# Performance work log

Measured on AMD Instinct MI355X. Metric: run time of the kernel, lower is better.

The kernel has to match this reference:

```python
import jax, jax.numpy as jnp
import numpy as np

D_MODEL = 768
HEAD = 12
D_K = D_MODEL // HEAD


def setup_inputs() -> dict:
    key = jax.random.key(0)
    ks = jax.random.split(key, 9)
    s = 1.0 / np.sqrt(D_MODEL)
    return {
        "x": jax.random.normal(ks[0], (2, 4096, D_MODEL), dtype=jnp.float32),
        "Wq": jax.random.normal(ks[1], (D_MODEL, D_MODEL), dtype=jnp.float32) * s,
        "bq": jax.random.normal(ks[2], (D_MODEL,), dtype=jnp.float32) * 0.01,
        "Wk": jax.random.normal(ks[3], (D_MODEL, D_MODEL), dtype=jnp.float32) * s,
        "bk": jax.random.normal(ks[4], (D_MODEL,), dtype=jnp.float32) * 0.01,
        "Wv": jax.random.normal(ks[5], (D_MODEL, D_MODEL), dtype=jnp.float32) * s,
        "bv": jax.random.normal(ks[6], (D_MODEL,), dtype=jnp.float32) * 0.01,
        "Wo": jax.random.normal(ks[7], (D_MODEL, D_MODEL), dtype=jnp.float32) * s,
        "bo": jax.random.normal(ks[8], (D_MODEL,), dtype=jnp.float32) * 0.01,
    }


def reference(x, Wq, bq, Wk, bk, Wv, bv, Wo, bo):
    B, S, _ = x.shape
    # Linear projections, split into heads: [B, H, S, d_k]
    def proj(W, b):
        return (x @ W + b).reshape(B, S, HEAD, D_K).transpose(0, 2, 1, 3)
    Q, K, V = proj(Wq, bq), proj(Wk, bk), proj(Wv, bv)
    scale = 1.0 / jnp.sqrt(jnp.asarray(D_K, x.dtype))
    # [B, H, S, S] attention scores (materialized, as in the original module)
    scores = jnp.einsum('bhqd,bhkd->bhqk', Q, K) * scale
    probs = jax.nn.softmax(scores, axis=-1)  # dropout is identity in eval mode
    ctx = jnp.einsum('bhqk,bhkd->bhqd', probs, V)
    ctx = ctx.transpose(0, 2, 1, 3).reshape(B, S, D_MODEL)
    return ctx @ Wo + bo
```

## Files before the change

### kernel.cpp

```cpp
#include <hip/hip_runtime.h>

#define D_MODEL 768
#define S_LEN   4096
#define NHEAD   12
#define DK      64
#define TKA     64

typedef _Float16 f16;
typedef _Float16 f16x8 __attribute__((ext_vector_type(8)));
typedef _Float16 f16x4 __attribute__((ext_vector_type(4)));
typedef __fp16   fp16x2 __attribute__((ext_vector_type(2)));
typedef float    f32x4 __attribute__((ext_vector_type(4)));

#define MFMA16(a, b, c) __builtin_amdgcn_mfma_f32_16x16x32_f16(a, b, c, 0, 0, 0)

#define Q_PRESCALE 0.18033688f
#define SOFTMAX_C  11.54156036f

__device__ inline f16x8 ldf(const f16* p) {
    return *reinterpret_cast<const f16x8*>(p);
}

__device__ inline void gl2lds16(const f16* g, f16* l) {
    __builtin_amdgcn_global_load_lds(
        (const __attribute__((address_space(1))) void*)g,
        (__attribute__((address_space(3))) void*)l, 16, 0, 0);
}

__global__ __launch_bounds__(256) void cvt_x_kernel(const float* __restrict__ x,
                                                    f16* __restrict__ xb) {
    size_t i = ((size_t)blockIdx.x * 256 + threadIdx.x) * 4;
    float4 v = *reinterpret_cast<const float4*>(x + i);
    f16x4 o = { (f16)v.x, (f16)v.y, (f16)v.z, (f16)v.w };
    *reinterpret_cast<f16x4*>(xb + i) = o;
}

__global__ __launch_bounds__(256) void wtrans_kernel(const float* __restrict__ Wq,
                                                     const float* __restrict__ Wk,
                                                     const float* __restrict__ Wv,
                                                     const float* __restrict__ Wo,
                                                     f16* __restrict__ WT) {
    const int z = blockIdx.z;
    const float* in = (z == 0) ? Wq : (z == 1) ? Wk : (z == 2) ? Wv : Wo;
    f16* out = WT + (size_t)z * D_MODEL * D_MODEL;
    __shared__ float tile[32][33];
    const int tx = threadIdx.x, ty = threadIdx.y;
    const int n0 = blockIdx.x * 32, k0 = blockIdx.y * 32;
#pragma unroll
    for (int j = 0; j < 32; j += 8)
        tile[ty + j][tx] = in[(size_t)(k0 + ty + j) * D_MODEL + n0 + tx];
    __syncthreads();
#pragma unroll
    for (int j = 0; j < 32; j += 8)
        out[(size_t)(n0 + ty + j) * D_MODEL + k0 + tx] = (f16)tile[tx][ty + j];
}

__global__ __launch_bounds__(256, 3) void gemm_qkv_kernel(
        const f16* __restrict__ A, const f16* __restrict__ WT,
        const float* __restrict__ bq, const float* __restrict__ bk,
        const float* __restrict__ bv,
        f16* __restrict__ Qb, f16* __restrict__ Kb, f16* __restrict__ Vt) {
    __shared__ __align__(16) f16 asmem[3][128 * 32];
    __shared__ __align__(16) f16 bsmem[3][128 * 32];
    const int z = blockIdx.z;
    const f16* Bt = WT + (size_t)z * D_MODEL * D_MODEL;
    const float* bias = (z == 0) ? bq : (z == 1) ? bk : bv;
    const int w = threadIdx.x >> 6;
    const int lane = threadIdx.x & 63;
    const int ln = lane & 15, quad = lane >> 4;
    const int mb = blockIdx.x * 128;
    const int nb = blockIdx.y * 128;
    const int mloc = (w & 1) * 64, nloc = (w >> 1) * 64;
    const int l0 = w * 64 + lane;

    auto stage = [&](int buf, int kb) {
#pragma unroll
        for (int p = 0; p < 2; p++) {
            const int l = p * 256 + l0;
            gl2lds16(A + (size_t)(mb + (l >> 2)) * D_MODEL + kb + (l & 3) * 8,
                     &asmem[buf][(p * 256 + w * 64) * 8]);
        }
#pragma unroll
        for (int p = 0; p < 2; p++) {
            const int l = p * 256 + l0;
            gl2lds16(Bt + (size_t)(nb + (l >> 2)) * D_MODEL + kb + (l & 3) * 8,
                     &bsmem[buf][(p * 256 + w * 64) * 8]);
        }
    };

    f32x4 acc[4][4] = {};
    stage(0, 0);
    stage(1, 32);
    __syncthreads();

    const int NIT = D_MODEL / 32;
    int cb = 0, sb = 2;
    for (int it = 0; it < NIT; ++it) {
        f16x8 af[4], bf[4];
#pragma unroll
        for (int i = 0; i < 4; i++)
            af[i] = ldf(&asmem[cb][(mloc + i * 16 + ln) * 32 + quad * 8]);
#pragma unroll
        for (int t = 0; t < 4; t++)
            bf[t] = ldf(&bsmem[cb][(nloc + t * 16 + ln) * 32 + quad * 8]);
#pragma unroll
        for (int i = 0; i < 4; i++)
#pragma unroll
            for (int t = 0; t < 4; t++)
                acc[i][t] = MFMA16(af[i], bf[t], acc[i][t]);
        __syncthreads();
        if (it + 2 < NIT) stage(sb, (it + 2) * 32);
        cb = (cb == 2) ? 0 : cb + 1;
        sb = (sb == 2) ? 0 : sb + 1;
    }

#pragma unroll
    for (int t = 0; t < 4; t++) {
        const int n = nb + nloc + t * 16 + ln;
        const float bval = bias[n];
        const int h = n >> 6, d = n & 63;
#pragma unroll
        for (int i = 0; i < 4; i++) {
            const int m = mb + mloc + i * 16 + quad * 4;
            const int b = m >> 12, s = m & 4095;
            const int bh = b * NHEAD + h;
            if (z == 0) {
#pragma unroll
                for (int r = 0; r < 4; r++)
                    Qb[((size_t)bh * S_LEN + s + r) * DK + d] =
                        (f16)((acc[i][t][r] + bval) * Q_PRESCALE);
            } else if (z == 1) {
#pragma unroll
                for (int r = 0; r < 4; r++)
                    Kb[((size_t)bh * S_LEN + s + r) * DK + d] =
                        (f16)(acc[i][t][r] + bval);
            } else {
                f16x4 pk;
#pragma unroll
                for (int r = 0; r < 4; r++) pk[r] = (f16)(acc[i][t][r] + bval);
                *reinterpret_cast<f16x4*>(&Vt[((size_t)bh * DK + d) * S_LEN + s]) = pk;
            }
        }
    }
}

__global__ __launch_bounds__(256, 3) void attn_kernel(const f16* __restrict__ Qb,
                                                      const f16* __restrict__ Kb,
                                                      const f16* __restrict__ Vt,
                                                      f16* __restrict__ Ctx) {
    __shared__ __align__(16) f16 kbuf[3][TKA * DK];
    __shared__ __align__(16) f16 vbuf[3][DK * TKA];

    const int w = threadIdx.x >> 6;
    const int lane = threadIdx.x & 63;
    const int ln = lane & 15, quad = lane >> 4;

    const int blk = blockIdx.x;
    const int xcd = blk & 7, sidx = blk >> 3;
    const int bh = xcd * 3 + (sidx >> 5);
    const int qb = (sidx & 31) * 128;
    const int b = bh / NHEAD, h = bh % NHEAD;

    const f16* Kbh = Kb + (size_t)bh * S_LEN * DK;
    const f16* Vbh = Vt + (size_t)bh * DK * S_LEN;

    f16x8 aq[2][2];
#pragma unroll
    for (int i2 = 0; i2 < 2; i2++) {
        const f16* qp = Qb + ((size_t)bh * S_LEN + qb + w * 32 + i2 * 16 + ln) * DK;
        aq[i2][0] = ldf(qp + quad * 8);
        aq[i2][1] = ldf(qp + 32 + quad * 8);
    }

    int rS[2], ckS[2], cvS[2];
#pragma unroll
    for (int p = 0; p < 2; p++) {
        const int l = p * 256 + w * 64 + lane;
        const int r = l >> 3;
        rS[p]  = r;
        ckS[p] = ((l & 7) - r - (r >> 2)) & 7;
        cvS[p] = ((l & 7) - r - (r >> 3)) & 7;
    }

    auto stage = [&](int buf, int kk) {
#pragma unroll
        for (int p = 0; p < 2; p++)
            gl2lds16(Kbh + (size_t)(kk + rS[p]) * DK + ckS[p] * 8,
                     &kbuf[buf][(p * 256 + w * 64) * 8]);
#pragma unroll
        for (int p = 0; p < 2; p++)
            gl2lds16(Vbh + (size_t)rS[p] * S_LEN + kk + cvS[p] * 8,
                     &vbuf[buf][(p * 256 + w * 64) * 8]);
    };

    f32x4 acc[4][2] = {};
    float lsum[2] = {0.f, 0.f};

    stage(0, 0);
    stage(1, TKA);
    __syncthreads();

    const int NIT = S_LEN / TKA;
    int cb = 0, sb = 2;
    for (int it = 0; it < NIT; ++it) {
        const f16* kb = kbuf[cb];
        const f16* vb = vbuf[cb];

        union { f16x8 v; fp16x2 h2[4]; } pb[2][2];

#pragma unroll
        for (int kt = 0; kt < 2; kt++) {
#pragma unroll
            for (int a = 0; a < 2; a++) {
                const int rr = kt * 32 + 8 * (ln >> 2) + 4 * a + (ln & 3);
                const int sw = rr + (rr >> 2);
                const f16x8 kf0 = ldf(kb + rr * DK + (((quad + sw) & 7) * 8));
                const f16x8 kf1 = ldf(kb + rr * DK + (((quad + 4 + sw) & 7) * 8));
#pragma unroll
                for (int i2 = 0; i2 < 2; i2++) {
                    f32x4 si = { -SOFTMAX_C, -SOFTMAX_C, -SOFTMAX_C, -SOFTMAX_C };
                    si = MFMA16(kf0, aq[i2][0], si);
                    si = MFMA16(kf1, aq[i2][1], si);
                    const float e0 = __builtin_amdgcn_exp2f(si[0]);
                    const float e1 = __builtin_amdgcn_exp2f(si[1]);
                    const float e2 = __builtin_amdgcn_exp2f(si[2]);
                    const float e3 = __builtin_amdgcn_exp2f(si[3]);
                    lsum[i2] += (e0 + e1) + (e2 + e3);
                    pb[kt][i2].h2[2 * a]     = __builtin_amdgcn_cvt_pkrtz(e0, e1);
                    pb[kt][i2].h2[2 * a + 1] = __builtin_amdgcn_cvt_pkrtz(e2, e3);
                }
            }
        }

#pragma unroll
        for (int t = 0; t < 4; t++) {
            const int rr = t * 16 + ln;
            const int sw = rr + (rr >> 3);
#pragma unroll
            for (int kt = 0; kt < 2; kt++) {
                const f16x8 vf = ldf(vb + rr * TKA + (((quad + 4 * kt + sw) & 7) * 8));
#pragma unroll
                for (int i2 = 0; i2 < 2; i2++)
                    acc[t][i2] = MFMA16(vf, pb[kt][i2].v, acc[t][i2]);
            }
        }

        __syncthreads();
        if (it + 2 < NIT) stage(sb, (it + 2) * TKA);
        cb = (cb == 2) ? 0 : cb + 1;
        sb = (sb == 2) ? 0 : sb + 1;
    }

#pragma unroll
    for (int i2 = 0; i2 < 2; i2++) {
        float l = lsum[i2];
        l += __shfl_xor(l, 16, 64);
        l += __shfl_xor(l, 32, 64);
        const float rl = 1.0f / l;
        const int q = qb + w * 32 + i2 * 16 + ln;
        f16* cp = Ctx + ((size_t)b * S_LEN + q) * D_MODEL + h * DK + 4 * quad;
#pragma unroll
        for (int t = 0; t < 4; t++) {
            f16x4 pk;
#pragma unroll
            for (int r = 0; r < 4; r++) pk[r] = (f16)(acc[t][i2][r] * rl);
            *reinterpret_cast<f16x4*>(cp + t * 16) = pk;
        }
    }
}

__global__ __launch_bounds__(256, 3) void gemm_o_kernel(const f16* __restrict__ A,
                                                        const f16* __restrict__ Bt,
                                                        const float* __restrict__ bo,
                                                        float* __restrict__ out) {
    __shared__ __align__(16) f16 asmem[3][128 * 32];
    __shared__ __align__(16) f16 bsmem[3][128 * 32];
    const int w = threadIdx.x >> 6;
    const int lane = threadIdx.x & 63;
    const int ln = lane & 15, quad = lane >> 4;
    const int mb = blockIdx.x * 128;
    const int nb = blockIdx.y * 128;
    const int mloc = (w & 1) * 64, nloc = (w >> 1) * 64;
    const int l0 = w * 64 + lane;

    auto stage = [&](int buf, int kb) {
#pragma unroll
        for (int p = 0; p < 2; p++) {
            const int l = p * 256 + l0;
            gl2lds16(A + (size_t)(mb + (l >> 2)) * D_MODEL + kb + (l & 3) * 8,
                     &asmem[buf][(p * 256 + w * 64) * 8]);
        }
#pragma unroll
        for (int p = 0; p < 2; p++) {
            const int l = p * 256 + l0;
            gl2lds16(Bt + (size_t)(nb + (l >> 2)) * D_MODEL + kb + (l & 3) * 8,
                     &bsmem[buf][(p * 256 + w * 64) * 8]);
        }
    };

    f32x4 acc[4][4] = {};
    stage(0, 0);
    stage(1, 32);
    __syncthreads();

    const int NIT = D_MODEL / 32;
    int cb = 0, sb = 2;
    for (int it = 0; it < NIT; ++it) {
        f16x8 af[4], bf[4];
#pragma unroll
        for (int i = 0; i < 4; i++)
            af[i] = ldf(&asmem[cb][(mloc + i * 16 + ln) * 32 + quad * 8]);
#pragma unroll
        for (int t = 0; t < 4; t++)
            bf[t] = ldf(&bsmem[cb][(nloc + t * 16 + ln) * 32 + quad * 8]);
#pragma unroll
        for (int i = 0; i < 4; i++)
#pragma unroll
            for (int t = 0; t < 4; t++)
                acc[i][t] = MFMA16(af[i], bf[t], acc[i][t]);
        __syncthreads();
        if (it + 2 < NIT) stage(sb, (it + 2) * 32);
        cb = (cb == 2) ? 0 : cb + 1;
        sb = (sb == 2) ? 0 : sb + 1;
    }

#pragma unroll
    for (int t = 0; t < 4; t++) {
        const int n = nb + nloc + t * 16 + ln;
        const float bval = bo[n];
#pragma unroll
        for (int i = 0; i < 4; i++) {
            const int m = mb + mloc + i * 16 + quad * 4;
#pragma unroll
            for (int r = 0; r < 4; r++)
                out[(size_t)(m + r) * D_MODEL + n] = acc[i][t][r] + bval;
        }
    }
}

extern "C" void kernel_launch(void* const* d_in, const int* in_sizes, int n_in,
                              void* d_out, int out_size, void* d_ws, size_t ws_size,
                              hipStream_t stream) {
    const float* x  = (const float*)d_in[0];
    const float* Wq = (const float*)d_in[1];
    const float* bq = (const float*)d_in[2];
    const float* Wk = (const float*)d_in[3];
    const float* bk = (const float*)d_in[4];
    const float* Wv = (const float*)d_in[5];
    const float* bv = (const float*)d_in[6];
    const float* Wo = (const float*)d_in[7];
    const float* bo = (const float*)d_in[8];
    float* out = (float*)d_out;

    f16* ws = (f16*)d_ws;
    f16* Xb  = ws;
    f16* Ctx = ws;
    f16* WT  = ws + 6291456;
    f16* Qb  = ws + 8650752;
    f16* Kb  = ws + 14942208;
    f16* Vt  = ws + 21233664;

    cvt_x_kernel<<<6144, 256, 0, stream>>>(x, Xb);
    wtrans_kernel<<<dim3(24, 24, 4), dim3(32, 8), 0, stream>>>(Wq, Wk, Wv, Wo, WT);
    gemm_qkv_kernel<<<dim3(64, 6, 3), 256, 0, stream>>>(Xb, WT, bq, bk, bv, Qb, Kb, Vt);
    attn_kernel<<<768, 256, 0, stream>>>(Qb, Kb, Vt, Ctx);
    gemm_o_kernel<<<dim3(64, 6), 256, 0, stream>>>(Ctx, WT + (size_t)3 * D_MODEL * D_MODEL, bo, out);
}
```

Baseline: 271.3 us.

## Switch to double-buffered LDS with static buffers and precomputed offsets

Replaces the triple-buffered LDS ring in the QKV GEMM, attention and output GEMM kernels with a double buffer. The loop is unrolled by two so buffer indices become compile-time constants, and global and LDS address offsets are precomputed outside the loop. The attention kernel also raises wave priority around the PV MFMAs and accumulates the row sum with packed float2 adds, and the QKV GEMM raises its occupancy hint to 4 blocks. The aim is less LDS and fewer registers so more blocks fit per CU, plus less per-iteration address arithmetic. The cost is a shorter prefetch distance: the next tile is issued only after a barrier, right after the previous compute, which may expose more memory latency.

```diff
diff --git a/kernel.cpp b/kernel.cpp
--- a/kernel.cpp
+++ b/kernel.cpp
@@ -11,6 +11,7 @@
 typedef _Float16 f16x4 __attribute__((ext_vector_type(4)));
 typedef __fp16   fp16x2 __attribute__((ext_vector_type(2)));
 typedef float    f32x4 __attribute__((ext_vector_type(4)));
+typedef float    f32x2 __attribute__((ext_vector_type(2)));
 
 #define MFMA16(a, b, c) __builtin_amdgcn_mfma_f32_16x16x32_f16(a, b, c, 0, 0, 0)
 
@@ -55,13 +56,13 @@
         out[(size_t)(n0 + ty + j) * D_MODEL + k0 + tx] = (f16)tile[tx][ty + j];
 }
 
-__global__ __launch_bounds__(256, 3) void gemm_qkv_kernel(
+__global__ __launch_bounds__(256, 4) void gemm_qkv_kernel(
         const f16* __restrict__ A, const f16* __restrict__ WT,
         const float* __restrict__ bq, const float* __restrict__ bk,
         const float* __restrict__ bv,
         f16* __restrict__ Qb, f16* __restrict__ Kb, f16* __restrict__ Vt) {
-    __shared__ __align__(16) f16 asmem[3][128 * 32];
-    __shared__ __align__(16) f16 bsmem[3][128 * 32];
+    __shared__ __align__(16) f16 asmem[2][128 * 32];
+    __shared__ __align__(16) f16 bsmem[2][128 * 32];
     const int z = blockIdx.z;
     const f16* Bt = WT + (size_t)z * D_MODEL * D_MODEL;
     const float* bias = (z == 0) ? bq : (z == 1) ? bk : bv;
@@ -73,45 +74,55 @@
     const int mloc = (w & 1) * 64, nloc = (w >> 1) * 64;
     const int l0 = w * 64 + lane;
 
+    const f16* aS[2];
+    const f16* bS[2];
+#pragma unroll
+    for (int p = 0; p < 2; p++) {
+        const int l = p * 256 + l0;
+        aS[p] = A  + (size_t)(mb + (l >> 2)) * D_MODEL + (l & 3) * 8;
+        bS[p] = Bt + (size_t)(nb + (l >> 2)) * D_MODEL + (l & 3) * 8;
+    }
     auto stage = [&](int buf, int kb) {
 #pragma unroll
-        for (int p = 0; p < 2; p++) {
-            const int l = p * 256 + l0;
-            gl2lds16(A + (size_t)(mb + (l >> 2)) * D_MODEL + kb + (l & 3) * 8,
-                     &asmem[buf][(p * 256 + w * 64) * 8]);
-        }
-#pragma unroll
-        for (int p = 0; p < 2; p++) {
-            const int l = p * 256 + l0;
-            gl2lds16(Bt + (size_t)(nb + (l >> 2)) * D_MODEL + kb + (l & 3) * 8,
-                     &bsmem[buf][(p * 256 + w * 64) * 8]);
-        }
-    };
+        for (int p = 0; p < 2; p++)
+            gl2lds16(aS[p] + kb, &asmem[buf][(p * 256 + w * 64) * 8]);
+#pragma unroll
+        for (int p = 0; p < 2; p++)
+            gl2lds16(bS[p] + kb, &bsmem[buf][(p * 256 + w * 64) * 8]);
+    };
+
+    int aoff[4], boff[4];
+#pragma unroll
+    for (int i = 0; i < 4; i++) aoff[i] = (mloc + i * 16 + ln) * 32 + quad * 8;
+#pragma unroll
+    for (int t = 0; t < 4; t++) boff[t] = (nloc + t * 16 + ln) * 32 + quad * 8;
 
     f32x4 acc[4][4] = {};
+    auto body = [&](const f16* as, const f16* bs) {
+        f16x8 af[4], bf[4];
+#pragma unroll
+        for (int i = 0; i < 4; i++) af[i] = ldf(as + aoff[i]);
+#pragma unroll
+        for (int t = 0; t < 4; t++) bf[t] = ldf(bs + boff[t]);
+#pragma unroll
+        for (int i = 0; i < 4; i++)
+#pragma unroll
+            for (int t = 0; t < 4; t++)
+                acc[i][t] = MFMA16(af[i], bf[t], acc[i][t]);
+    };
+
     stage(0, 0);
     stage(1, 32);
     __syncthreads();
 
-    const int NIT = D_MODEL / 32;
-    int cb = 0, sb = 2;
-    for (int it = 0; it < NIT; ++it) {
-        f16x8 af[4], bf[4];
-#pragma unroll
-        for (int i = 0; i < 4; i++)
-            af[i] = ldf(&asmem[cb][(mloc + i * 16 + ln) * 32 + quad * 8]);
-#pragma unroll
-        for (int t = 0; t < 4; t++)
-            bf[t] = ldf(&bsmem[cb][(nloc + t * 16 + ln) * 32 + quad * 8]);
-#pragma unroll
-        for (int i = 0; i < 4; i++)
-#pragma unroll
-            for (int t = 0; t < 4; t++)
-                acc[i][t] = MFMA16(af[i], bf[t], acc[i][t]);
-        __syncthreads();
-        if (it + 2 < NIT) stage(sb, (it + 2) * 32);
-        cb = (cb == 2) ? 0 : cb + 1;
-        sb = (sb == 2) ? 0 : sb + 1;
+#pragma unroll 1
+    for (int j = 0; j < 12; ++j) {
+        body(asmem[0], bsmem[0]);
+        __syncthreads();
+        if (j < 11) stage(0, (2 * j + 2) * 32);
+        body(asmem[1], bsmem[1]);
+        __syncthreads();
+        if (j < 11) stage(1, (2 * j + 3) * 32);
     }
 
 #pragma unroll
@@ -148,8 +159,8 @@
                                                       const f16* __restrict__ Kb,
                                                       const f16* __restrict__ Vt,
                                                       f16* __restrict__ Ctx) {
-    __shared__ __align__(16) f16 kbuf[3][TKA * DK];
-    __shared__ __align__(16) f16 vbuf[3][DK * TKA];
+    __shared__ __align__(16) f16 kbuf[2][TKA * DK];
+    __shared__ __align__(16) f16 vbuf[2][DK * TKA];
 
     const int w = threadIdx.x >> 6;
     const int lane = threadIdx.x & 63;
@@ -172,88 +183,108 @@
         aq[i2][1] = ldf(qp + 32 + quad * 8);
     }
 
-    int rS[2], ckS[2], cvS[2];
+    const f16* kS[2];
+    const f16* vS[2];
 #pragma unroll
     for (int p = 0; p < 2; p++) {
         const int l = p * 256 + w * 64 + lane;
         const int r = l >> 3;
-        rS[p]  = r;
-        ckS[p] = ((l & 7) - r - (r >> 2)) & 7;
-        cvS[p] = ((l & 7) - r - (r >> 3)) & 7;
+        const int ck = ((l & 7) - r - (r >> 2)) & 7;
+        const int cv = ((l & 7) - r - (r >> 3)) & 7;
+        kS[p] = Kbh + (size_t)r * DK + ck * 8;
+        vS[p] = Vbh + (size_t)r * S_LEN + cv * 8;
     }
 
     auto stage = [&](int buf, int kk) {
 #pragma unroll
         for (int p = 0; p < 2; p++)
-            gl2lds16(Kbh + (size_t)(kk + rS[p]) * DK + ckS[p] * 8,
-                     &kbuf[buf][(p * 256 + w * 64) * 8]);
-#pragma unroll
-        for (int p = 0; p < 2; p++)
-            gl2lds16(Vbh + (size_t)rS[p] * S_LEN + kk + cvS[p] * 8,
-                     &vbuf[buf][(p * 256 + w * 64) * 8]);
-    };
-
+            gl2lds16(kS[p] + (size_t)kk * DK, &kbuf[buf][(p * 256 + w * 64) * 8]);
+#pragma unroll
+        for (int p = 0; p < 2; p++)
+            gl2lds16(vS[p] + kk, &vbuf[buf][(p * 256 + w * 64) * 8]);
+    };
+
+    int koff[2][2][2];
+#pragma unroll
+    for (int kt = 0; kt < 2; kt++)
+#pragma unroll
+        for (int a = 0; a < 2; a++) {
+            const int rr = kt * 32 + 8 * (ln >> 2) + 4 * a + (ln & 3);
+            const int sw = rr + (rr >> 2);
+            koff[kt][a][0] = rr * DK + (((quad + sw) & 7) * 8);
+            koff[kt][a][1] = rr * DK + (((quad + 4 + sw) & 7) * 8);
+        }
+    int voff[4][2];
+#pragma unroll
+    for (int t = 0; t < 4; t++) {
+        const int rr = t * 16 + ln;
+        const int sw = rr + (rr >> 3);
+#pragma unroll
+        for (int kt = 0; kt < 2; kt++)
+            voff[t][kt] = rr * TKA + (((quad + 4 * kt + sw) & 7) * 8);
+    }
+
+    const f32x4 cinit = { -SOFTMAX_C, -SOFTMAX_C, -SOFTMAX_C, -SOFTMAX_C };
     f32x4 acc[4][2] = {};
-    float lsum[2] = {0.f, 0.f};
-
-    stage(0, 0);
-    stage(1, TKA);
-    __syncthreads();
-
-    const int NIT = S_LEN / TKA;
-    int cb = 0, sb = 2;
-    for (int it = 0; it < NIT; ++it) {
-        const f16* kb = kbuf[cb];
-        const f16* vb = vbuf[cb];
-
+    f32x2 lsum2[2] = {};
+
+    auto compute = [&](const f16* kb, const f16* vb) {
         union { f16x8 v; fp16x2 h2[4]; } pb[2][2];
 
 #pragma unroll
         for (int kt = 0; kt < 2; kt++) {
 #pragma unroll
             for (int a = 0; a < 2; a++) {
-                const int rr = kt * 32 + 8 * (ln >> 2) + 4 * a + (ln & 3);
-                const int sw = rr + (rr >> 2);
-                const f16x8 kf0 = ldf(kb + rr * DK + (((quad + sw) & 7) * 8));
-                const f16x8 kf1 = ldf(kb + rr * DK + (((quad + 4 + sw) & 7) * 8));
+                const f16x8 kf0 = ldf(kb + koff[kt][a][0]);
+                const f16x8 kf1 = ldf(kb + koff[kt][a][1]);
 #pragma unroll
                 for (int i2 = 0; i2 < 2; i2++) {
-                    f32x4 si = { -SOFTMAX_C, -SOFTMAX_C, -SOFTMAX_C, -SOFTMAX_C };
-                    si = MFMA16(kf0, aq[i2][0], si);
+                    f32x4 si = MFMA16(kf0, aq[i2][0], cinit);
                     si = MFMA16(kf1, aq[i2][1], si);
                     const float e0 = __builtin_amdgcn_exp2f(si[0]);
                     const float e1 = __builtin_amdgcn_exp2f(si[1]);
                     const float e2 = __builtin_amdgcn_exp2f(si[2]);
                     const float e3 = __builtin_amdgcn_exp2f(si[3]);
-                    lsum[i2] += (e0 + e1) + (e2 + e3);
+                    f32x2 ea = { e0, e1 };
+                    f32x2 eb = { e2, e3 };
+                    lsum2[i2] += ea + eb;
                     pb[kt][i2].h2[2 * a]     = __builtin_amdgcn_cvt_pkrtz(e0, e1);
                     pb[kt][i2].h2[2 * a + 1] = __builtin_amdgcn_cvt_pkrtz(e2, e3);
                 }
             }
         }
 
+        __builtin_amdgcn_s_setprio(1);
 #pragma unroll
         for (int t = 0; t < 4; t++) {
-            const int rr = t * 16 + ln;
-            const int sw = rr + (rr >> 3);
 #pragma unroll
             for (int kt = 0; kt < 2; kt++) {
-                const f16x8 vf = ldf(vb + rr * TKA + (((quad + 4 * kt + sw) & 7) * 8));
+                const f16x8 vf = ldf(vb + voff[t][kt]);
 #pragma unroll
                 for (int i2 = 0; i2 < 2; i2++)
                     acc[t][i2] = MFMA16(vf, pb[kt][i2].v, acc[t][i2]);
             }
         }
-
-        __syncthreads();
-        if (it + 2 < NIT) stage(sb, (it + 2) * TKA);
-        cb = (cb == 2) ? 0 : cb + 1;
-        sb = (sb == 2) ? 0 : sb + 1;
+        __builtin_amdgcn_s_setprio(0);
+    };
+
+    stage(0, 0);
+    stage(1, TKA);
+    __syncthreads();
+
+#pragma unroll 1
+    for (int j = 0; j < 32; ++j) {
+        compute(kbuf[0], vbuf[0]);
+        __syncthreads();
+        if (j < 31) stage(0, (2 * j + 2) * TKA);
+        compute(kbuf[1], vbuf[1]);
+        __syncthreads();
+        if (j < 31) stage(1, (2 * j + 3) * TKA);
     }
 
 #pragma unroll
     for (int i2 = 0; i2 < 2; i2++) {
-        float l = lsum[i2];
+        float l = lsum2[i2][0] + lsum2[i2][1];
         l += __shfl_xor(l, 16, 64);
         l += __shfl_xor(l, 32, 64);
         const float rl = 1.0f / l;
@@ -273,8 +304,8 @@
                                                         const f16* __restrict__ Bt,
                                                         const float* __restrict__ bo,
                                                         float* __restrict__ out) {
-    __shared__ __align__(16) f16 asmem[3][128 * 32];
-    __shared__ __align__(16) f16 bsmem[3][128 * 32];
+    __shared__ __align__(16) f16 asmem[2][128 * 32];
+    __shared__ __align__(16) f16 bsmem[2][128 * 32];
     const int w = threadIdx.x >> 6;
     const int lane = threadIdx.x & 63;
     const int ln = lane & 15, quad = lane >> 4;
@@ -283,45 +314,55 @@
     const int mloc = (w & 1) * 64, nloc = (w >> 1) * 64;
     const int l0 = w * 64 + lane;
 
+    const f16* aS[2];
+    const f16* bS[2];
+#pragma unroll
+    for (int p = 0; p < 2; p++) {
+        const int l = p * 256 + l0;
+        aS[p] = A  + (size_t)(mb + (l >> 2)) * D_MODEL + (l & 3) * 8;
+        bS[p] = Bt + (size_t)(nb + (l >> 2)) * D_MODEL + (l & 3) * 8;
+    }
     auto stage = [&](int buf, int kb) {
 #pragma unroll
-        for (int p = 0; p < 2; p++) {
-            const int l = p * 256 + l0;
-            gl2lds16(A + (size_t)(mb + (l >> 2)) * D_MODEL + kb + (l & 3) * 8,
-                     &asmem[buf][(p * 256 + w * 64) * 8]);
-        }
-#pragma unroll
-        for (int p = 0; p < 2; p++) {
-            const int l = p * 256 + l0;
-            gl2lds16(Bt + (size_t)(nb + (l >> 2)) * D_MODEL + kb + (l & 3) * 8,
-                     &bsmem[buf][(p * 256 + w * 64) * 8]);
-        }
-    };
+        for (int p = 0; p < 2; p++)
+            gl2lds16(aS[p] + kb, &asmem[buf][(p * 256 + w * 64) * 8]);
+#pragma unroll
+        for (int p = 0; p < 2; p++)
+            gl2lds16(bS[p] + kb, &bsmem[buf][(p * 256 + w * 64) * 8]);
+    };
+
+    int aoff[4], boff[4];
+#pragma unroll
+    for (int i = 0; i < 4; i++) aoff[i] = (mloc + i * 16 + ln) * 32 + quad * 8;
+#pragma unroll
+    for (int t = 0; t < 4; t++) boff[t] = (nloc + t * 16 + ln) * 32 + quad * 8;
 
     f32x4 acc[4][4] = {};
+    auto body = [&](const f16* as, const f16* bs) {
+        f16x8 af[4], bf[4];
+#pragma unroll
+        for (int i = 0; i < 4; i++) af[i] = ldf(as + aoff[i]);
+#pragma unroll
+        for (int t = 0; t < 4; t++) bf[t] = ldf(bs + boff[t]);
+#pragma unroll
+        for (int i = 0; i < 4; i++)
+#pragma unroll
+            for (int t = 0; t < 4; t++)
+                acc[i][t] = MFMA16(af[i], bf[t], acc[i][t]);
+    };
+
     stage(0, 0);
     stage(1, 32);
     __syncthreads();
 
-    const int NIT = D_MODEL / 32;
-    int cb = 0, sb = 2;
-    for (int it = 0; it < NIT; ++it) {
-        f16x8 af[4], bf[4];
-#pragma unroll
-        for (int i = 0; i < 4; i++)
-            af[i] = ldf(&asmem[cb][(mloc + i * 16 + ln) * 32 + quad * 8]);
-#pragma unroll
-        for (int t = 0; t < 4; t++)
-            bf[t] = ldf(&bsmem[cb][(nloc + t * 16 + ln) * 32 + quad * 8]);
-#pragma unroll
-        for (int i = 0; i < 4; i++)
-#pragma unroll
-            for (int t = 0; t < 4; t++)
-                acc[i][t] = MFMA16(af[i], bf[t], acc[i][t]);
-        __syncthreads();
-        if (it + 2 < NIT) stage(sb, (it + 2) * 32);
-        cb = (cb == 2) ? 0 : cb + 1;
-        sb = (sb == 2) ? 0 : sb + 1;
+#pragma unroll 1
+    for (int j = 0; j < 12; ++j) {
+        body(asmem[0], bsmem[0]);
+        __syncthreads();
+        if (j < 11) stage(0, (2 * j + 2) * 32);
+        body(asmem[1], bsmem[1]);
+        __syncthreads();
+        if (j < 11) stage(1, (2 * j + 3) * 32);
     }
 
 #pragma unroll
```

Result: slower. 323.0 us (+19.1%).

## Load K fragments directly into registers with two-deep prefetch, dropping K LDS staging

Applied to the files above, without the earlier changes.

The attention kernel no longer stages K tiles through shared memory. Each lane loads its K MFMA fragments straight from global memory into registers, double-buffered (kA/kB) two iterations ahead. The loop is unrolled by two to alternate register buffers, V offsets are precomputed, and s_setprio raises priority around the PV MFMA block. This removes LDS traffic and LDS reads for K, and frees shared memory. In exchange it adds 16 f16x8 registers per lane and issues uncoalesced global loads that could hurt occupancy under launch_bounds(256,3).

```diff
diff --git a/kernel.cpp b/kernel.cpp
--- a/kernel.cpp
+++ b/kernel.cpp
@@ -148,7 +148,6 @@
                                                       const f16* __restrict__ Kb,
                                                       const f16* __restrict__ Vt,
                                                       f16* __restrict__ Ctx) {
-    __shared__ __align__(16) f16 kbuf[3][TKA * DK];
     __shared__ __align__(16) f16 vbuf[3][DK * TKA];
 
     const int w = threadIdx.x >> 6;
@@ -172,84 +171,114 @@
         aq[i2][1] = ldf(qp + 32 + quad * 8);
     }
 
-    int rS[2], ckS[2], cvS[2];
+    int koffg[8];
+#pragma unroll
+    for (int kt = 0; kt < 2; kt++)
+#pragma unroll
+        for (int a = 0; a < 2; a++) {
+            const int rr = kt * 32 + 8 * (ln >> 2) + 4 * a + (ln & 3);
+            koffg[(kt * 2 + a) * 2 + 0] = rr * DK + quad * 8;
+            koffg[(kt * 2 + a) * 2 + 1] = rr * DK + 32 + quad * 8;
+        }
+
+#define LOADK(KARR, kk)                                                      \
+    {                                                                        \
+        const f16* kb_ = Kbh + (size_t)(kk) * DK;                            \
+        _Pragma("unroll")                                                    \
+        for (int i_ = 0; i_ < 8; ++i_) KARR[i_] = ldf(kb_ + koffg[i_]);      \
+    }
+
+    int rS[2], cvS[2];
 #pragma unroll
     for (int p = 0; p < 2; p++) {
         const int l = p * 256 + w * 64 + lane;
         const int r = l >> 3;
         rS[p]  = r;
-        ckS[p] = ((l & 7) - r - (r >> 2)) & 7;
         cvS[p] = ((l & 7) - r - (r >> 3)) & 7;
     }
 
     auto stage = [&](int buf, int kk) {
-#pragma unroll
-        for (int p = 0; p < 2; p++)
-            gl2lds16(Kbh + (size_t)(kk + rS[p]) * DK + ckS[p] * 8,
-                     &kbuf[buf][(p * 256 + w * 64) * 8]);
 #pragma unroll
         for (int p = 0; p < 2; p++)
             gl2lds16(Vbh + (size_t)rS[p] * S_LEN + kk + cvS[p] * 8,
                      &vbuf[buf][(p * 256 + w * 64) * 8]);
     };
 
+    int voff[4][2];
+#pragma unroll
+    for (int t = 0; t < 4; t++) {
+        const int rr = t * 16 + ln;
+        const int sw = rr + (rr >> 3);
+#pragma unroll
+        for (int kt = 0; kt < 2; kt++)
+            voff[t][kt] = rr * TKA + (((quad + 4 * kt + sw) & 7) * 8);
+    }
+
+    const f32x4 cinit = { -SOFTMAX_C, -SOFTMAX_C, -SOFTMAX_C, -SOFTMAX_C };
     f32x4 acc[4][2] = {};
     float lsum[2] = {0.f, 0.f};
 
+    f16x8 kA[8], kB[8];
+    const int NIT = S_LEN / TKA;
+
     stage(0, 0);
     stage(1, TKA);
+    LOADK(kA, 0);
+    LOADK(kB, TKA);
     __syncthreads();
 
-    const int NIT = S_LEN / TKA;
     int cb = 0, sb = 2;
-    for (int it = 0; it < NIT; ++it) {
-        const f16* kb = kbuf[cb];
-        const f16* vb = vbuf[cb];
-
-        union { f16x8 v; fp16x2 h2[4]; } pb[2][2];
-
-#pragma unroll
-        for (int kt = 0; kt < 2; kt++) {
-#pragma unroll
-            for (int a = 0; a < 2; a++) {
-                const int rr = kt * 32 + 8 * (ln >> 2) + 4 * a + (ln & 3);
-                const int sw = rr + (rr >> 2);
-                const f16x8 kf0 = ldf(kb + rr * DK + (((quad + sw) & 7) * 8));
-                const f16x8 kf1 = ldf(kb + rr * DK + (((quad + 4 + sw) & 7) * 8));
-#pragma unroll
-                for (int i2 = 0; i2 < 2; i2++) {
-                    f32x4 si = { -SOFTMAX_C, -SOFTMAX_C, -SOFTMAX_C, -SOFTMAX_C };
-                    si = MFMA16(kf0, aq[i2][0], si);
-                    si = MFMA16(kf1, aq[i2][1], si);
-                    const float e0 = __builtin_amdgcn_exp2f(si[0]);
-                    const float e1 = __builtin_amdgcn_exp2f(si[1]);
-                    const float e2 = __builtin_amdgcn_exp2f(si[2]);
-                    const float e3 = __builtin_amdgcn_exp2f(si[3]);
-                    lsum[i2] += (e0 + e1) + (e2 + e3);
-                    pb[kt][i2].h2[2 * a]     = __builtin_amdgcn_cvt_pkrtz(e0, e1);
-                    pb[kt][i2].h2[2 * a + 1] = __builtin_amdgcn_cvt_pkrtz(e2, e3);
-                }
-            }
-        }
-
-#pragma unroll
-        for (int t = 0; t < 4; t++) {
-            const int rr = t * 16 + ln;
-            const int sw = rr + (rr >> 3);
-#pragma unroll
-            for (int kt = 0; kt < 2; kt++) {
-                const f16x8 vf = ldf(vb + rr * TKA + (((quad + 4 * kt + sw) & 7) * 8));
-#pragma unroll
-                for (int i2 = 0; i2 < 2; i2++)
-                    acc[t][i2] = MFMA16(vf, pb[kt][i2].v, acc[t][i2]);
-            }
-        }
-
-        __syncthreads();
-        if (it + 2 < NIT) stage(sb, (it + 2) * TKA);
-        cb = (cb == 2) ? 0 : cb + 1;
-        sb = (sb == 2) ? 0 : sb + 1;
-    }
+
+#define ATTN_STEP(KARR, itv)                                                 \
+    {                                                                        \
+        const f16* vb = vbuf[cb];                                            \
+        union { f16x8 v; fp16x2 h2[4]; } pb[2][2];                           \
+        _Pragma("unroll")                                                    \
+        for (int kt = 0; kt < 2; kt++) {                                     \
+            _Pragma("unroll")                                                \
+            for (int a = 0; a < 2; a++) {                                    \
+                const f16x8 kf0 = KARR[(kt * 2 + a) * 2 + 0];                \
+                const f16x8 kf1 = KARR[(kt * 2 + a) * 2 + 1];                \
+                _Pragma("unroll")                                            \
+                for (int i2 = 0; i2 < 2; i2++) {                             \
+                    f32x4 si = MFMA16(kf0, aq[i2][0], cinit);                \
+                    si = MFMA16(kf1, aq[i2][1], si);                         \
+                    const float e0 = __builtin_amdgcn_exp2f(si[0]);          \
+                    const float e1 = __builtin_amdgcn_exp2f(si[1]);          \
+                    const float e2 = __builtin_amdgcn_exp2f(si[2]);          \
+                    const float e3 = __builtin_amdgcn_exp2f(si[3]);          \
+                    lsum[i2] += (e0 + e1) + (e2 + e3);                       \
+                    pb[kt][i2].h2[2 * a]     = __builtin_amdgcn_cvt_pkrtz(e0, e1); \
+                    pb[kt][i2].h2[2 * a + 1] = __builtin_amdgcn_cvt_pkrtz(e2, e3); \
+                }                                                            \
+            }                                                                \
+        }                                                                    \
+        if ((itv) + 2 < NIT) LOADK(KARR, ((itv) + 2) * TKA);                 \
+        __builtin_amdgcn_s_setprio(1);                                       \
+        _Pragma("unroll")                                                    \
+        for (int t = 0; t < 4; t++) {                                        \
+            _Pragma("unroll")                                                \
+            for (int kt = 0; kt < 2; kt++) {                                 \
+                const f16x8 vf = ldf(vb + voff[t][kt]);                      \
+                _Pragma("unroll")                                            \
+                for (int i2 = 0; i2 < 2; i2++)                               \
+                    acc[t][i2] = MFMA16(vf, pb[kt][i2].v, acc[t][i2]);       \
+            }                                                                \
+        }                                                                    \
+        __builtin_amdgcn_s_setprio(0);                                       \
+        __syncthreads();                                                     \
+        if ((itv) + 2 < NIT) stage(sb, ((itv) + 2) * TKA);                   \
+        cb = (cb == 2) ? 0 : cb + 1;                                         \
+        sb = (sb == 2) ? 0 : sb + 1;                                         \
+    }
+
+#pragma unroll 1
+    for (int j = 0; j < NIT / 2; ++j) {
+        ATTN_STEP(kA, 2 * j);
+        ATTN_STEP(kB, 2 * j + 1);
+    }
+#undef ATTN_STEP
+#undef LOADK
 
 #pragma unroll
     for (int i2 = 0; i2 < 2; i2++) {
```

New measurement: 697.2 us. 157% more time.
